# Kernel optimization log

Measured on AMD Instinct MI355X. Metric: run time of the kernel, lower is better.

## Reference

```python
import jax, jax.numpy as jnp
import numpy as np
from jax import lax

A_NUM = 2
N_LAYER = 4
DIM0 = 64   # fr_inner_dim_0 == signal_dim_0 (forced by view/squeeze logic)
DIM1 = 256  # fr_inner_dim_1
SD0 = 64
SD1 = 64
K_OUT = 8
UPS = 4
EPS = 1e-5
BSZ = 64


def setup_inputs() -> dict:
    key = jax.random.key(0)
    ks = jax.random.split(key, 16)
    s = 0.05
    f32 = jnp.float32
    inp = jax.random.normal(ks[0], (BSZ, 2, SD0, SD1), f32)
    # ComplexConv2d2 weights stored squeezed to their effective matmul form.
    W_in_r = jax.random.normal(ks[1], (DIM1 * A_NUM, SD1), f32) * s
    W_in_i = jax.random.normal(ks[2], (DIM1 * A_NUM, SD1), f32) * s
    W_pre_r = jax.random.normal(ks[3], (A_NUM,), f32) * s
    W_pre_i = jax.random.normal(ks[4], (A_NUM,), f32) * s
    Wm_r = jax.random.normal(ks[5], (2 * N_LAYER, SD0, SD0), f32) * s
    Wm_i = jax.random.normal(ks[6], (2 * N_LAYER, SD0, SD0), f32) * s
    Wc_r = jax.random.normal(ks[7], (N_LAYER, A_NUM), f32) * s
    Wc_i = jax.random.normal(ks[8], (N_LAYER, A_NUM), f32) * s
    W_l3_r = jax.random.normal(ks[9], (DIM0 * A_NUM, SD0), f32) * s
    W_l3_i = jax.random.normal(ks[10], (DIM0 * A_NUM, SD0), f32) * s
    conv1_w = jax.random.normal(ks[11], (N_LAYER, A_NUM, A_NUM, 3, 3), f32) * s
    conv2_w = jax.random.normal(ks[12], (N_LAYER, A_NUM, A_NUM, 3, 3), f32) * s
    bn1_g = jnp.ones((N_LAYER, A_NUM), f32)
    bn1_b = jnp.zeros((N_LAYER, A_NUM), f32)
    bn2_g = jnp.ones((N_LAYER, A_NUM), f32)
    bn2_b = jnp.zeros((N_LAYER, A_NUM), f32)
    W_out = jax.random.normal(ks[13], (A_NUM, 1, K_OUT, K_OUT), f32) * s
    return {"inp": inp, "W_in_r": W_in_r, "W_in_i": W_in_i, "W_pre_r": W_pre_r,
            "W_pre_i": W_pre_i, "Wm_r": Wm_r, "Wm_i": Wm_i, "Wc_r": Wc_r,
            "Wc_i": Wc_i, "W_l3_r": W_l3_r, "W_l3_i": W_l3_i,
            "conv1_w": conv1_w, "bn1_g": bn1_g, "bn1_b": bn1_b,
            "conv2_w": conv2_w, "bn2_g": bn2_g, "bn2_b": bn2_b, "W_out": W_out}


def _circ_conv(x, w):
    xp = jnp.pad(x, ((0, 0), (0, 0), (1, 1), (1, 1)), mode='wrap')
    return lax.conv_general_dilated(xp, w, (1, 1), 'VALID',
                                    dimension_numbers=('NCHW', 'OIHW', 'NCHW'))


def _bn(x, g, b):
    mu = jnp.mean(x, axis=(0, 2, 3), keepdims=True)
    var = jnp.var(x, axis=(0, 2, 3), keepdims=True)
    return (x - mu) * lax.rsqrt(var + EPS) * g[None, :, None, None] + b[None, :, None, None]


def _forward(inp, W_in_r, W_in_i, W_pre_r, W_pre_i, Wm_r, Wm_i, Wc_r, Wc_i,
             W_l3_r, W_l3_i, conv1_w, bn1_g, bn1_b, conv2_w, bn2_g, bn2_b, W_out):
    bsz = inp.shape[0]
    xr, xi = inp[:, 0], inp[:, 1]  # (b, sd0, sd1)
    # input_layer: complex conv, kernel (1, sd1) -> contraction over width
    yr = jnp.einsum('bhw,cw->bch', xr, W_in_r) - jnp.einsum('bhw,cw->bch', xi, W_in_i)
    yi = jnp.einsum('bhw,cw->bch', xi, W_in_r) + jnp.einsum('bhw,cw->bch', xr, W_in_i)
    xreal = yr.reshape(bsz, A_NUM, DIM1, DIM0).transpose(0, 1, 3, 2)  # (b,A,dim0,dim1)
    ximag = yi.reshape(bsz, A_NUM, DIM1, DIM0).transpose(0, 1, 3, 2)
    # concat_pre: complex 1x1 conv, A_NUM -> 1 channel
    x_real = (jnp.einsum('bahw,a->bhw', xreal, W_pre_r) - jnp.einsum('bahw,a->bhw', ximag, W_pre_i))[:, None]
    x_imag = (jnp.einsum('bahw,a->bhw', ximag, W_pre_r) + jnp.einsum('bahw,a->bhw', xreal, W_pre_i))[:, None]
    Gr, Gi = x_real, x_imag  # loop-invariant Gnk

    def phase_branch(xr_, xi_, Wr, Wi):
        a, c = xr_[:, 0], xi_[:, 0]  # (b, dim0, dim1)
        # complex conv kernel (sd0,1) == matmul over height
        Ir = (jnp.einsum('bhw,ch->bcw', a, Wr) - jnp.einsum('bhw,ch->bcw', c, Wi))[:, None]
        Ii = (jnp.einsum('bhw,ch->bcw', c, Wr) + jnp.einsum('bhw,ch->bcw', a, Wi))[:, None]
        s_ = 1.0 + jnp.log(Ir * Ir + Ii * Ii)
        EIr, EIi = s_ * Ir, -s_ * Ii
        ur, ui = Wr.T, Wi.T
        zr = jnp.einsum('hc,bncw->bnhw', ur, EIr) - jnp.einsum('hc,bncw->bnhw', ui, EIi)
        zi = jnp.einsum('hc,bncw->bnhw', ur, EIi) + jnp.einsum('hc,bncw->bnhw', ui, EIr)
        wr = jnp.sum(Gr * zr - Gi * zi, axis=3)  # (b,1,dim0)
        wi = jnp.sum(Gr * zi + Gi * zr, axis=3)
        ang = jnp.arctan2(wi, wr)[..., None]  # broadcast over dim1
        cr, ci = jnp.cos(ang), -jnp.sin(ang)
        return Gr * cr - Gi * ci, Gr * ci + Gi * cr

    for i in range(N_LAYER):
        x1r, x1i = phase_branch(x_real, x_imag, Wm_r[i], Wm_i[i])
        x2r, x2i = phase_branch(x_real, x_imag, Wm_r[i + N_LAYER], Wm_i[i + N_LAYER])
        sr = jnp.concatenate([x1r, x2r], 1)
        si = jnp.concatenate([x1i, x2i], 1)
        x_real = (jnp.einsum('bahw,a->bhw', sr, Wc_r[i]) - jnp.einsum('bahw,a->bhw', si, Wc_i[i]))[:, None]
        x_imag = (jnp.einsum('bahw,a->bhw', si, Wc_r[i]) + jnp.einsum('bahw,a->bhw', sr, Wc_i[i]))[:, None]

    # input_layer3: complex conv kernel (sd0,1), 1 -> dim0*A_NUM channels
    a, c = x_real[:, 0], x_imag[:, 0]
    fr = (jnp.einsum('bhw,ch->bcw', a, W_l3_r) - jnp.einsum('bhw,ch->bcw', c, W_l3_i)).reshape(bsz, -1)
    fi = (jnp.einsum('bhw,ch->bcw', c, W_l3_r) + jnp.einsum('bhw,ch->bcw', a, W_l3_i)).reshape(bsz, -1)
    m = jnp.max(jnp.sqrt(fr * fr + fi * fi), axis=1, keepdims=True)
    fr, fi = fr / m, fi / m
    fr = fr.reshape(bsz, A_NUM, DIM0, DIM1)
    fi = fi.reshape(bsz, A_NUM, DIM0, DIM1)
    x = jnp.sqrt(fr * fr + fi * fi)

    for i in range(N_LAYER):
        h = jax.nn.relu(_bn(_circ_conv(x, conv1_w[i]), bn1_g[i], bn1_b[i]))
        h = _bn(_circ_conv(h, conv2_w[i]), bn2_g[i], bn2_b[i])
        x = jax.nn.relu(x + h)

    # ConvTranspose2d(A_NUM, 1, K_OUT, stride=UPS, padding=2, output_padding=1)
    wt = jnp.flip(W_out, (2, 3)).transpose(1, 0, 2, 3)  # (1, A_NUM, k, k)
    pad_lo = K_OUT - 1 - 2
    pad_hi = pad_lo + 1
    y = lax.conv_general_dilated(x, wt, (1, 1),
                                 [(pad_lo, pad_hi), (pad_lo, pad_hi)],
                                 lhs_dilation=(UPS, UPS),
                                 dimension_numbers=('NCHW', 'OIHW', 'NCHW'))
    return y[:, 0]


def reference(inp, W_in_r, W_in_i, W_pre_r, W_pre_i, Wm_r, Wm_i, Wc_r, Wc_i,
              W_l3_r, W_l3_i, conv1_w, bn1_g, bn1_b, conv2_w, bn2_g, bn2_b, W_out):
    return _forward(inp, W_in_r, W_in_i, W_pre_r, W_pre_i, Wm_r, Wm_i, Wc_r, Wc_i,
                    W_l3_r, W_l3_i, conv1_w, bn1_g, bn1_b, conv2_w, bn2_g, bn2_b, W_out)
```

## Files before the change

kernel.cpp:

```cpp
#include <hip/hip_runtime.h>
#include <hip/hip_bf16.h>
#include <math.h>


__global__ void k0_prep(const float* __restrict__ Wr, const float* __restrict__ Wi,
                        const float* __restrict__ pr, const float* __restrict__ pi,
                        float* __restrict__ ArT, float* __restrict__ AiT,
                        float2* __restrict__ C) {
    int w  = blockIdx.x;
    int w2 = threadIdx.x;
    float p0r = pr[0], p1r = pr[1], p0i = pi[0], p1i = pi[1];
    float wr0 = Wr[w2 * 64 + w],         wi0 = Wi[w2 * 64 + w];
    float wr1 = Wr[(256 + w2) * 64 + w], wi1 = Wi[(256 + w2) * 64 + w];
    ArT[w * 256 + w2] = p0r * wr0 - p0i * wi0 + p1r * wr1 - p1i * wi1;
    AiT[w * 256 + w2] = p0r * wi0 + p0i * wr0 + p1r * wi1 + p1i * wr1;
    if (w2 < 64) C[w * 64 + w2] = make_float2(1.f, 0.f);
}

__global__ void k0b_T(const float* __restrict__ Wmr, const float* __restrict__ Wmi,
                      float* __restrict__ WmrT, float* __restrict__ WmiT) {
    int m = blockIdx.x;
    int t = threadIdx.x;
    const float* sr = Wmr + m * 4096;
    const float* si = Wmi + m * 4096;
    float* dr = WmrT + m * 4096;
    float* di = WmiT + m * 4096;
    for (int k = t; k < 4096; k += 256) {
        int c = k >> 6, h = k & 63;
        dr[h * 64 + c] = sr[k];
        di[h * 64 + c] = si[k];
    }
}

__global__ __launch_bounds__(256) void k1_G(const float* __restrict__ inp,
                                            const float* __restrict__ ArT,
                                            const float* __restrict__ AiT,
                                            float* __restrict__ Gr, float* __restrict__ Gi) {
    int hc = blockIdx.x;
    int b  = blockIdx.y;
    int t  = threadIdx.x;
    __shared__ float sxr[8][64], sxi[8][64];
    int base_r = (b * 2 + 0) * 4096 + hc * 8 * 64;
    int base_i = (b * 2 + 1) * 4096 + hc * 8 * 64;
    for (int k = t; k < 512; k += 256) {
        int r = k >> 6, w = k & 63;
        sxr[r][w] = inp[base_r + r * 64 + w];
        sxi[r][w] = inp[base_i + r * 64 + w];
    }
    __syncthreads();
    float accr[8], acci[8];
#pragma unroll
    for (int r = 0; r < 8; r++) { accr[r] = 0.f; acci[r] = 0.f; }
    for (int k = 0; k < 64; k++) {
        float ar = ArT[k * 256 + t], ai = AiT[k * 256 + t];
#pragma unroll
        for (int r = 0; r < 8; r++) {
            float xr = sxr[r][k], xi = sxi[r][k];
            accr[r] += xr * ar - xi * ai;
            acci[r] += xi * ar + xr * ai;
        }
    }
#pragma unroll
    for (int r = 0; r < 8; r++) {
        int h = hc * 8 + r;
        Gr[(b * 64 + h) * 256 + t] = accr[r];
        Gi[(b * 64 + h) * 256 + t] = acci[r];
    }
}

__global__ __launch_bounds__(1024) void k2_layer(const float* __restrict__ Gr,
                                                 const float* __restrict__ Gi,
                                                 const float2* __restrict__ C,
                                                 const float* __restrict__ Wmr,
                                                 const float* __restrict__ Wmi,
                                                 const float* __restrict__ WmrT,
                                                 const float* __restrict__ WmiT,
                                                 float2* __restrict__ wsum, int layer) {
    int wc = blockIdx.x;
    int j  = blockIdx.y;
    int b  = blockIdx.z;
    int t = threadIdx.x, tx = t & 63, ty = t >> 6;
    __shared__ float2 sX[4096];
    int mat = layer + 4 * j;
    int c0 = __builtin_amdgcn_readfirstlane(ty << 2);
    const float* Wr0  = Wmr  + mat * 4096 + c0 * 64;
    const float* Wi0  = Wmi  + mat * 4096 + c0 * 64;
    const float* WrT0 = WmrT + mat * 4096 + c0 * 64;
    const float* WiT0 = WmiT + mat * 4096 + c0 * 64;

    int gbase = b * 16384 + wc * 64 + tx;
    float gr_[4], gi_[4];
#pragma unroll
    for (int r = 0; r < 4; r++) {
        int h = (ty << 2) + r;
        float gr = Gr[gbase + h * 256], gi = Gi[gbase + h * 256];
        gr_[r] = gr; gi_[r] = gi;
        float2 c = C[b * 64 + h];
        sX[h * 64 + tx] = make_float2(c.x * gr - c.y * gi, c.x * gi + c.y * gr);
    }
    __syncthreads();

    float Ir[4] = {0.f, 0.f, 0.f, 0.f}, Ii[4] = {0.f, 0.f, 0.f, 0.f};
#pragma unroll 8
    for (int h = 0; h < 64; h++) {
        float2 x = sX[h * 64 + tx];
#pragma unroll
        for (int r = 0; r < 4; r++) {
            float wr = Wr0[r * 64 + h], wi = Wi0[r * 64 + h];
            Ir[r] += wr * x.x - wi * x.y;
            Ii[r] += wr * x.y + wi * x.x;
        }
    }
    __syncthreads();
#pragma unroll
    for (int r = 0; r < 4; r++) {
        float m2 = Ir[r] * Ir[r] + Ii[r] * Ii[r];
        float s = 1.f + __logf(m2);
        sX[((ty << 2) + r) * 64 + tx] = make_float2(s * Ir[r], -s * Ii[r]);
    }
    __syncthreads();

    float Zr[4] = {0.f, 0.f, 0.f, 0.f}, Zi[4] = {0.f, 0.f, 0.f, 0.f};
#pragma unroll 8
    for (int c = 0; c < 64; c++) {
        float2 e = sX[c * 64 + tx];
#pragma unroll
        for (int r = 0; r < 4; r++) {
            float wr = WrT0[r * 64 + c], wi = WiT0[r * 64 + c];
            Zr[r] += wr * e.x - wi * e.y;
            Zi[r] += wr * e.y + wi * e.x;
        }
    }
#pragma unroll
    for (int r = 0; r < 4; r++) {
        int h = (ty << 2) + r;
        float pr = gr_[r] * Zr[r] - gi_[r] * Zi[r];
        float pi = gr_[r] * Zi[r] + gi_[r] * Zr[r];
#pragma unroll
        for (int off = 32; off > 0; off >>= 1) {
            pr += __shfl_xor(pr, off);
            pi += __shfl_xor(pi, off);
        }
        if (tx == 0) wsum[((b * 64 + h) * 2 + j) * 4 + wc] = make_float2(pr, pi);
    }
}

__global__ void k3_cupdate(const float2* __restrict__ wsum, float2* __restrict__ C,
                           const float* __restrict__ Wcr, const float* __restrict__ Wci,
                           int layer) {
    int id = blockIdx.x * 256 + threadIdx.x;
    float accr = 0.f, acci = 0.f;
#pragma unroll
    for (int j = 0; j < 2; j++) {
        float wr = 0.f, wi = 0.f;
#pragma unroll
        for (int wc = 0; wc < 4; wc++) {
            float2 p = wsum[(id * 2 + j) * 4 + wc];
            wr += p.x; wi += p.y;
        }
        float m2 = wr * wr + wi * wi;
        float cr, ci;
        if (m2 > 0.f) {
            float inv = 1.f / sqrtf(m2);
            cr = wr * inv; ci = -wi * inv;
        } else { cr = 1.f; ci = 0.f; }
        float wcr = Wcr[layer * 2 + j], wci = Wci[layer * 2 + j];
        accr += cr * wcr - ci * wci;
        acci += ci * wcr + cr * wci;
    }
    C[id] = make_float2(accr, acci);
}

__global__ __launch_bounds__(1024) void k4_proj(const float* __restrict__ Gr,
                                                const float* __restrict__ Gi,
                                                const float2* __restrict__ C,
                                                const float* __restrict__ W3r,
                                                const float* __restrict__ W3i,
                                                float* __restrict__ xmag,
                                                float* __restrict__ pmax) {
    int wc = blockIdx.x;
    int cb = blockIdx.y;
    int b  = blockIdx.z;
    int t = threadIdx.x, tx = t & 63, ty = t >> 6;
    __shared__ float2 sX[4096];
    int c0 = __builtin_amdgcn_readfirstlane(ty << 2);
    const float* W3r0 = W3r + (cb * 64 + c0) * 64;
    const float* W3i0 = W3i + (cb * 64 + c0) * 64;
    int gbase = b * 16384 + wc * 64 + tx;
#pragma unroll
    for (int r = 0; r < 4; r++) {
        int h = (ty << 2) + r;
        float gr = Gr[gbase + h * 256], gi = Gi[gbase + h * 256];
        float2 c = C[b * 64 + h];
        sX[h * 64 + tx] = make_float2(c.x * gr - c.y * gi, c.x * gi + c.y * gr);
    }
    __syncthreads();
    float Fr[4] = {0.f, 0.f, 0.f, 0.f}, Fi[4] = {0.f, 0.f, 0.f, 0.f};
#pragma unroll 8
    for (int h = 0; h < 64; h++) {
        float2 x = sX[h * 64 + tx];
#pragma unroll
        for (int r = 0; r < 4; r++) {
            float wr = W3r0[r * 64 + h], wi = W3i0[r * 64 + h];
            Fr[r] += wr * x.x - wi * x.y;
            Fi[r] += wr * x.y + wi * x.x;
        }
    }
    float mx = 0.f;
#pragma unroll
    for (int r = 0; r < 4; r++) {
        int cl = (ty << 2) + r;
        float mag = sqrtf(Fr[r] * Fr[r] + Fi[r] * Fi[r]);
        xmag[(b * 128 + cb * 64 + cl) * 256 + wc * 64 + tx] = mag;
        mx = fmaxf(mx, mag);
    }
#pragma unroll
    for (int off = 32; off > 0; off >>= 1) mx = fmaxf(mx, __shfl_xor(mx, off));
    __syncthreads();
    float* scratch = (float*)sX;
    if (tx == 0) scratch[ty] = mx;
    __syncthreads();
    if (t == 0) {
        float m = scratch[0];
#pragma unroll
        for (int k = 1; k < 16; k++) m = fmaxf(m, scratch[k]);
        pmax[b * 8 + cb * 4 + wc] = m;
    }
}

__global__ void k5b_scale(float* __restrict__ x, const float* __restrict__ pmax) {
    int id = blockIdx.x * 256 + threadIdx.x;
    int b = id >> 15;
    float m = 0.f;
#pragma unroll
    for (int k = 0; k < 8; k++) m = fmaxf(m, pmax[b * 8 + k]);
    x[id] *= 1.f / m;
}

__global__ __launch_bounds__(256) void k_conv(const float* __restrict__ xin,
                                              const float* __restrict__ cw,
                                              const float* __restrict__ stats,
                                              float* __restrict__ hout,
                                              float* __restrict__ psum,
                                              float* __restrict__ psumsq,
                                              int layer, int apply_bn_relu) {
    int hb = blockIdx.x;
    int co = blockIdx.y;
    int b  = blockIdx.z;
    int tx = threadIdx.x;
    float wgt[18];
    const float* wp = cw + layer * 36 + co * 18;
#pragma unroll
    for (int k = 0; k < 18; k++) wgt[k] = wp[k];
    float sc0 = 1.f, sc1 = 1.f, sh0 = 0.f, sh1 = 0.f;
    if (apply_bn_relu) { sc0 = stats[0]; sc1 = stats[1]; sh0 = stats[2]; sh1 = stats[3]; }
    int wm = (tx + 255) & 255, wpp = (tx + 1) & 255;
    float lsum = 0.f, lsq = 0.f;
    for (int r = 0; r < 4; r++) {
        int hh = hb * 4 + r;
        int hm = (hh + 63) & 63, hp = (hh + 1) & 63;
        const int rows[3] = {hm, hh, hp};
        const int cols[3] = {wm, tx, wpp};
        float acc = 0.f;
#pragma unroll
        for (int ci = 0; ci < 2; ci++) {
            const float* xp = xin + (b * 2 + ci) * 16384;
            float sc = ci ? sc1 : sc0, sh = ci ? sh1 : sh0;
            const float* wg = wgt + ci * 9;
#pragma unroll
            for (int kh = 0; kh < 3; kh++)
#pragma unroll
                for (int kw = 0; kw < 3; kw++) {
                    float v = xp[rows[kh] * 256 + cols[kw]];
                    if (apply_bn_relu) v = fmaxf(v * sc + sh, 0.f);
                    acc += wg[kh * 3 + kw] * v;
                }
        }
        hout[((b * 2 + co) * 64 + hh) * 256 + tx] = acc;
        lsum += acc; lsq += acc * acc;
    }
#pragma unroll
    for (int off = 32; off > 0; off >>= 1) {
        lsum += __shfl_xor(lsum, off);
        lsq  += __shfl_xor(lsq, off);
    }
    __shared__ float ssum[4], ssq[4];
    int ty = tx >> 6, lane = tx & 63;
    if (lane == 0) { ssum[ty] = lsum; ssq[ty] = lsq; }
    __syncthreads();
    if (tx == 0) {
        int bl = b * 16 + hb;
        psum[co * 1024 + bl]   = ssum[0] + ssum[1] + ssum[2] + ssum[3];
        psumsq[co * 1024 + bl] = ssq[0] + ssq[1] + ssq[2] + ssq[3];
    }
}

__global__ void k_stats(const float* __restrict__ psum, const float* __restrict__ psumsq,
                        const float* __restrict__ g, const float* __restrict__ bb,
                        float* __restrict__ stats, int layer) {
    int ch = threadIdx.x >> 6, lane = threadIdx.x & 63;
    float s = 0.f, q = 0.f;
    for (int k = lane; k < 1024; k += 64) { s += psum[ch * 1024 + k]; q += psumsq[ch * 1024 + k]; }
#pragma unroll
    for (int off = 32; off > 0; off >>= 1) { s += __shfl_xor(s, off); q += __shfl_xor(q, off); }
    if (lane == 0) {
        const float N = 1048576.f;
        float mu = s / N;
        float var = q / N - mu * mu;
        float rs = rsqrtf(var + 1e-5f);
        float gamma = g[layer * 2 + ch];
        stats[ch]     = rs * gamma;
        stats[2 + ch] = bb[layer * 2 + ch] - mu * rs * gamma;
    }
}

__global__ void k8_res(float* __restrict__ x, const float* __restrict__ h2,
                       const float* __restrict__ stats) {
    int id = blockIdx.x * 256 + threadIdx.x;
    int ch = (id >> 14) & 1;
    float v = x[id] + h2[id] * stats[ch] + stats[2 + ch];
    x[id] = fmaxf(v, 0.f);
}

__global__ void k9_out(const float* __restrict__ x, const float* __restrict__ Wout,
                       float* __restrict__ out) {
    const int TOT = 64 * 257 * 1025;
    int id = blockIdx.x * 256 + threadIdx.x;
    if (id >= TOT) return;
    int b   = id / 263425;
    int rem = id - b * 263425;
    int oh  = rem / 1025;
    int ow  = rem - oh * 1025;
    int kh0 = (5 - oh) & 3;
    int kw0 = (5 - ow) & 3;
    float acc = 0.f;
#pragma unroll
    for (int ah = 0; ah < 2; ah++) {
        int kh = kh0 + 4 * ah;
        int d = oh + kh - 5;
        if (d < 0 || d > 252) continue;
        int rh = d >> 2;
#pragma unroll
        for (int aw = 0; aw < 2; aw++) {
            int kw = kw0 + 4 * aw;
            int e = ow + kw - 5;
            if (e < 0 || e > 1020) continue;
            int rw = e >> 2;
#pragma unroll
            for (int ci = 0; ci < 2; ci++) {
                float wv = Wout[ci * 64 + (7 - kh) * 8 + (7 - kw)];
                acc += wv * x[((b * 2 + ci) * 64 + rh) * 256 + rw];
            }
        }
    }
    out[id] = acc;
}

extern "C" void kernel_launch(void* const* d_in, const int* in_sizes, int n_in,
                              void* d_out, int out_size, void* d_ws, size_t ws_size,
                              hipStream_t stream) {
    const float* inp   = (const float*)d_in[0];
    const float* Winr  = (const float*)d_in[1];
    const float* Wini  = (const float*)d_in[2];
    const float* Wprer = (const float*)d_in[3];
    const float* Wprei = (const float*)d_in[4];
    const float* Wmr   = (const float*)d_in[5];
    const float* Wmi   = (const float*)d_in[6];
    const float* Wcr   = (const float*)d_in[7];
    const float* Wci   = (const float*)d_in[8];
    const float* W3r   = (const float*)d_in[9];
    const float* W3i   = (const float*)d_in[10];
    const float* cw1   = (const float*)d_in[11];
    const float* bn1g  = (const float*)d_in[12];
    const float* bn1b  = (const float*)d_in[13];
    const float* cw2   = (const float*)d_in[14];
    const float* bn2g  = (const float*)d_in[15];
    const float* bn2b  = (const float*)d_in[16];
    const float* Wout  = (const float*)d_in[17];
    float* out = (float*)d_out;

    float* ws = (float*)d_ws;
    float*  ArT   = ws;
    float*  AiT   = ArT + 16384;
    float2* C     = (float2*)(AiT + 16384);
    float*  Gr    = (float*)C + 8192;
    float*  Gi    = Gr + 1048576;
    float2* wsum  = (float2*)(Gi + 1048576);
    float*  xmag  = (float*)wsum + 65536;
    float*  h2    = xmag + 2097152;
    float*  pmax  = h2 + 2097152;
    float*  psum1 = pmax + 512;
    float*  psq1  = psum1 + 2048;
    float*  psum2 = psq1 + 2048;
    float*  psq2  = psum2 + 2048;
    float*  stats = psq2 + 2048;
    float*  h1    = Gr;
    float*  WmrT  = h2;
    float*  WmiT  = h2 + 32768;

    k0_prep<<<64, 256, 0, stream>>>(Winr, Wini, Wprer, Wprei, ArT, AiT, C);
    k0b_T<<<8, 256, 0, stream>>>(Wmr, Wmi, WmrT, WmiT);
    k1_G<<<dim3(8, 64), 256, 0, stream>>>(inp, ArT, AiT, Gr, Gi);
    for (int i = 0; i < 4; i++) {
        k2_layer<<<dim3(4, 2, 64), 1024, 0, stream>>>(Gr, Gi, C, Wmr, Wmi, WmrT, WmiT, wsum, i);
        k3_cupdate<<<16, 256, 0, stream>>>(wsum, C, Wcr, Wci, i);
    }
    k4_proj<<<dim3(4, 2, 64), 1024, 0, stream>>>(Gr, Gi, C, W3r, W3i, xmag, pmax);
    k5b_scale<<<8192, 256, 0, stream>>>(xmag, pmax);
    for (int i = 0; i < 4; i++) {
        k_conv<<<dim3(16, 2, 64), 256, 0, stream>>>(xmag, cw1, stats, h1, psum1, psq1, i, 0);
        k_stats<<<1, 128, 0, stream>>>(psum1, psq1, bn1g, bn1b, stats, i);
        k_conv<<<dim3(16, 2, 64), 256, 0, stream>>>(h1, cw2, stats, h2, psum2, psq2, i, 1);
        k_stats<<<1, 128, 0, stream>>>(psum2, psq2, bn2g, bn2b, stats + 4, i);
        k8_res<<<8192, 256, 0, stream>>>(xmag, h2, stats + 4);
    }
    k9_out<<<65857, 256, 0, stream>>>(xmag, Wout, out);
}
```

Before: 591.0 us.

## Fuse scale and residual passes into conv kernels; merge k2 matrix pair per block

The separate max-normalisation kernel and the per-layer residual+ReLU kernel are removed. Their arithmetic is now applied on the fly where the next conv1 or the final transposed conv reads the activations, and conv1 writes the updated x into a ping-pong buffer that borrows the output array as scratch. k2_layer now processes both Wm matrices (j loop) in one 512-thread block with 8 rows per thread and a second shared buffer, so each G tile is loaded once instead of twice. The aim is to cut elementwise memory passes and kernel launches, at the cost of extra global reads inside the 3x3 stencil (the residual term is recomputed per tap) and higher register pressure in k2.

```diff
diff --git a/kernel.cpp b/kernel.cpp
--- a/kernel.cpp
+++ b/kernel.cpp
@@ -68,31 +68,26 @@
     }
 }
 
-__global__ __launch_bounds__(1024) void k2_layer(const float* __restrict__ Gr,
-                                                 const float* __restrict__ Gi,
-                                                 const float2* __restrict__ C,
-                                                 const float* __restrict__ Wmr,
-                                                 const float* __restrict__ Wmi,
-                                                 const float* __restrict__ WmrT,
-                                                 const float* __restrict__ WmiT,
-                                                 float2* __restrict__ wsum, int layer) {
+__global__ __launch_bounds__(512) void k2_layer(const float* __restrict__ Gr,
+                                                const float* __restrict__ Gi,
+                                                const float2* __restrict__ C,
+                                                const float* __restrict__ Wmr,
+                                                const float* __restrict__ Wmi,
+                                                const float* __restrict__ WmrT,
+                                                const float* __restrict__ WmiT,
+                                                float2* __restrict__ wsum, int layer) {
     int wc = blockIdx.x;
-    int j  = blockIdx.y;
-    int b  = blockIdx.z;
+    int b  = blockIdx.y;
     int t = threadIdx.x, tx = t & 63, ty = t >> 6;
     __shared__ float2 sX[4096];
-    int mat = layer + 4 * j;
-    int c0 = __builtin_amdgcn_readfirstlane(ty << 2);
-    const float* Wr0  = Wmr  + mat * 4096 + c0 * 64;
-    const float* Wi0  = Wmi  + mat * 4096 + c0 * 64;
-    const float* WrT0 = WmrT + mat * 4096 + c0 * 64;
-    const float* WiT0 = WmiT + mat * 4096 + c0 * 64;
+    __shared__ float2 sE[4096];
+    int h0 = __builtin_amdgcn_readfirstlane(ty << 3);
 
     int gbase = b * 16384 + wc * 64 + tx;
-    float gr_[4], gi_[4];
-#pragma unroll
-    for (int r = 0; r < 4; r++) {
-        int h = (ty << 2) + r;
+    float gr_[8], gi_[8];
+#pragma unroll
+    for (int r = 0; r < 8; r++) {
+        int h = h0 + r;
         float gr = Gr[gbase + h * 256], gi = Gi[gbase + h * 256];
         gr_[r] = gr; gi_[r] = gi;
         float2 c = C[b * 64 + h];
@@ -100,48 +95,56 @@
     }
     __syncthreads();
 
-    float Ir[4] = {0.f, 0.f, 0.f, 0.f}, Ii[4] = {0.f, 0.f, 0.f, 0.f};
-#pragma unroll 8
-    for (int h = 0; h < 64; h++) {
-        float2 x = sX[h * 64 + tx];
-#pragma unroll
-        for (int r = 0; r < 4; r++) {
-            float wr = Wr0[r * 64 + h], wi = Wi0[r * 64 + h];
-            Ir[r] += wr * x.x - wi * x.y;
-            Ii[r] += wr * x.y + wi * x.x;
-        }
-    }
-    __syncthreads();
-#pragma unroll
-    for (int r = 0; r < 4; r++) {
-        float m2 = Ir[r] * Ir[r] + Ii[r] * Ii[r];
-        float s = 1.f + __logf(m2);
-        sX[((ty << 2) + r) * 64 + tx] = make_float2(s * Ir[r], -s * Ii[r]);
-    }
-    __syncthreads();
-
-    float Zr[4] = {0.f, 0.f, 0.f, 0.f}, Zi[4] = {0.f, 0.f, 0.f, 0.f};
-#pragma unroll 8
-    for (int c = 0; c < 64; c++) {
-        float2 e = sX[c * 64 + tx];
-#pragma unroll
-        for (int r = 0; r < 4; r++) {
-            float wr = WrT0[r * 64 + c], wi = WiT0[r * 64 + c];
-            Zr[r] += wr * e.x - wi * e.y;
-            Zi[r] += wr * e.y + wi * e.x;
-        }
-    }
-#pragma unroll
-    for (int r = 0; r < 4; r++) {
-        int h = (ty << 2) + r;
-        float pr = gr_[r] * Zr[r] - gi_[r] * Zi[r];
-        float pi = gr_[r] * Zi[r] + gi_[r] * Zr[r];
-#pragma unroll
-        for (int off = 32; off > 0; off >>= 1) {
-            pr += __shfl_xor(pr, off);
-            pi += __shfl_xor(pi, off);
-        }
-        if (tx == 0) wsum[((b * 64 + h) * 2 + j) * 4 + wc] = make_float2(pr, pi);
+    for (int j = 0; j < 2; j++) {
+        int mat = layer + 4 * j;
+        const float* Wr0  = Wmr  + mat * 4096 + h0 * 64;
+        const float* Wi0  = Wmi  + mat * 4096 + h0 * 64;
+        const float* WrT0 = WmrT + mat * 4096 + h0 * 64;
+        const float* WiT0 = WmiT + mat * 4096 + h0 * 64;
+
+        float Ir[8] = {0,0,0,0,0,0,0,0}, Ii[8] = {0,0,0,0,0,0,0,0};
+#pragma unroll 4
+        for (int h = 0; h < 64; h++) {
+            float2 x = sX[h * 64 + tx];
+#pragma unroll
+            for (int r = 0; r < 8; r++) {
+                float wr = Wr0[r * 64 + h], wi = Wi0[r * 64 + h];
+                Ir[r] += wr * x.x - wi * x.y;
+                Ii[r] += wr * x.y + wi * x.x;
+            }
+        }
+#pragma unroll
+        for (int r = 0; r < 8; r++) {
+            float m2 = Ir[r] * Ir[r] + Ii[r] * Ii[r];
+            float s = 1.f + __logf(m2);
+            sE[(h0 + r) * 64 + tx] = make_float2(s * Ir[r], -s * Ii[r]);
+        }
+        __syncthreads();
+
+        float Zr[8] = {0,0,0,0,0,0,0,0}, Zi[8] = {0,0,0,0,0,0,0,0};
+#pragma unroll 4
+        for (int c = 0; c < 64; c++) {
+            float2 e = sE[c * 64 + tx];
+#pragma unroll
+            for (int r = 0; r < 8; r++) {
+                float wr = WrT0[r * 64 + c], wi = WiT0[r * 64 + c];
+                Zr[r] += wr * e.x - wi * e.y;
+                Zi[r] += wr * e.y + wi * e.x;
+            }
+        }
+#pragma unroll
+        for (int r = 0; r < 8; r++) {
+            int h = h0 + r;
+            float pr = gr_[r] * Zr[r] - gi_[r] * Zi[r];
+            float pi = gr_[r] * Zi[r] + gi_[r] * Zr[r];
+#pragma unroll
+            for (int off = 32; off > 0; off >>= 1) {
+                pr += __shfl_xor(pr, off);
+                pi += __shfl_xor(pi, off);
+            }
+            if (tx == 0) wsum[((b * 64 + h) * 2 + j) * 4 + wc] = make_float2(pr, pi);
+        }
+        __syncthreads();
     }
 }
 
@@ -195,7 +198,7 @@
         sX[h * 64 + tx] = make_float2(c.x * gr - c.y * gi, c.x * gi + c.y * gr);
     }
     __syncthreads();
-    float Fr[4] = {0.f, 0.f, 0.f, 0.f}, Fi[4] = {0.f, 0.f, 0.f, 0.f};
+    float Fr[4] = {0,0,0,0}, Fi[4] = {0,0,0,0};
 #pragma unroll 8
     for (int h = 0; h < 64; h++) {
         float2 x = sX[h * 64 + tx];
@@ -228,22 +231,16 @@
     }
 }
 
-__global__ void k5b_scale(float* __restrict__ x, const float* __restrict__ pmax) {
-    int id = blockIdx.x * 256 + threadIdx.x;
-    int b = id >> 15;
-    float m = 0.f;
-#pragma unroll
-    for (int k = 0; k < 8; k++) m = fmaxf(m, pmax[b * 8 + k]);
-    x[id] *= 1.f / m;
-}
-
-__global__ __launch_bounds__(256) void k_conv(const float* __restrict__ xin,
-                                              const float* __restrict__ cw,
-                                              const float* __restrict__ stats,
-                                              float* __restrict__ hout,
-                                              float* __restrict__ psum,
-                                              float* __restrict__ psumsq,
-                                              int layer, int apply_bn_relu) {
+__global__ __launch_bounds__(256) void k_conv1f(const float* __restrict__ xin,
+                                                const float* __restrict__ h2,
+                                                const float* __restrict__ cw,
+                                                const float* __restrict__ stats2,
+                                                const float* __restrict__ pmax,
+                                                float* __restrict__ hout,
+                                                float* __restrict__ xout,
+                                                float* __restrict__ psum,
+                                                float* __restrict__ psumsq,
+                                                int layer) {
     int hb = blockIdx.x;
     int co = blockIdx.y;
     int b  = blockIdx.z;
@@ -252,8 +249,15 @@
     const float* wp = cw + layer * 36 + co * 18;
 #pragma unroll
     for (int k = 0; k < 18; k++) wgt[k] = wp[k];
-    float sc0 = 1.f, sc1 = 1.f, sh0 = 0.f, sh1 = 0.f;
-    if (apply_bn_relu) { sc0 = stats[0]; sc1 = stats[1]; sh0 = stats[2]; sh1 = stats[3]; }
+    float sc0 = 0.f, sc1 = 0.f, sh0 = 0.f, sh1 = 0.f, inv = 1.f;
+    if (layer == 0) {
+        float m = 0.f;
+#pragma unroll
+        for (int k = 0; k < 8; k++) m = fmaxf(m, pmax[b * 8 + k]);
+        inv = 1.f / m;
+    } else {
+        sc0 = stats2[0]; sc1 = stats2[1]; sh0 = stats2[2]; sh1 = stats2[3];
+    }
     int wm = (tx + 255) & 255, wpp = (tx + 1) & 255;
     float lsum = 0.f, lsq = 0.f;
     for (int r = 0; r < 4; r++) {
@@ -264,15 +268,20 @@
         float acc = 0.f;
 #pragma unroll
         for (int ci = 0; ci < 2; ci++) {
-            const float* xp = xin + (b * 2 + ci) * 16384;
+            const float* xp  = xin + (b * 2 + ci) * 16384;
+            const float* hp2 = h2  + (b * 2 + ci) * 16384;
             float sc = ci ? sc1 : sc0, sh = ci ? sh1 : sh0;
             const float* wg = wgt + ci * 9;
 #pragma unroll
             for (int kh = 0; kh < 3; kh++)
 #pragma unroll
                 for (int kw = 0; kw < 3; kw++) {
-                    float v = xp[rows[kh] * 256 + cols[kw]];
-                    if (apply_bn_relu) v = fmaxf(v * sc + sh, 0.f);
+                    int idx = rows[kh] * 256 + cols[kw];
+                    float v;
+                    if (layer == 0) v = xp[idx] * inv;
+                    else            v = fmaxf(xp[idx] + hp2[idx] * sc + sh, 0.f);
+                    if (ci == co && kh == 1 && kw == 1)
+                        xout[(b * 2 + co) * 16384 + hh * 256 + tx] = v;
                     acc += wg[kh * 3 + kw] * v;
                 }
         }
@@ -285,8 +294,64 @@
         lsq  += __shfl_xor(lsq, off);
     }
     __shared__ float ssum[4], ssq[4];
-    int ty = tx >> 6, lane = tx & 63;
-    if (lane == 0) { ssum[ty] = lsum; ssq[ty] = lsq; }
+    int tyy = tx >> 6, lane = tx & 63;
+    if (lane == 0) { ssum[tyy] = lsum; ssq[tyy] = lsq; }
+    __syncthreads();
+    if (tx == 0) {
+        int bl = b * 16 + hb;
+        psum[co * 1024 + bl]   = ssum[0] + ssum[1] + ssum[2] + ssum[3];
+        psumsq[co * 1024 + bl] = ssq[0] + ssq[1] + ssq[2] + ssq[3];
+    }
+}
+
+__global__ __launch_bounds__(256) void k_conv2(const float* __restrict__ h1,
+                                               const float* __restrict__ cw,
+                                               const float* __restrict__ stats1,
+                                               float* __restrict__ hout,
+                                               float* __restrict__ psum,
+                                               float* __restrict__ psumsq,
+                                               int layer) {
+    int hb = blockIdx.x;
+    int co = blockIdx.y;
+    int b  = blockIdx.z;
+    int tx = threadIdx.x;
+    float wgt[18];
+    const float* wp = cw + layer * 36 + co * 18;
+#pragma unroll
+    for (int k = 0; k < 18; k++) wgt[k] = wp[k];
+    float sc0 = stats1[0], sc1 = stats1[1], sh0 = stats1[2], sh1 = stats1[3];
+    int wm = (tx + 255) & 255, wpp = (tx + 1) & 255;
+    float lsum = 0.f, lsq = 0.f;
+    for (int r = 0; r < 4; r++) {
+        int hh = hb * 4 + r;
+        int hm = (hh + 63) & 63, hp = (hh + 1) & 63;
+        const int rows[3] = {hm, hh, hp};
+        const int cols[3] = {wm, tx, wpp};
+        float acc = 0.f;
+#pragma unroll
+        for (int ci = 0; ci < 2; ci++) {
+            const float* xp = h1 + (b * 2 + ci) * 16384;
+            float sc = ci ? sc1 : sc0, sh = ci ? sh1 : sh0;
+            const float* wg = wgt + ci * 9;
+#pragma unroll
+            for (int kh = 0; kh < 3; kh++)
+#pragma unroll
+                for (int kw = 0; kw < 3; kw++) {
+                    float v = fmaxf(xp[rows[kh] * 256 + cols[kw]] * sc + sh, 0.f);
+                    acc += wg[kh * 3 + kw] * v;
+                }
+        }
+        hout[((b * 2 + co) * 64 + hh) * 256 + tx] = acc;
+        lsum += acc; lsq += acc * acc;
+    }
+#pragma unroll
+    for (int off = 32; off > 0; off >>= 1) {
+        lsum += __shfl_xor(lsum, off);
+        lsq  += __shfl_xor(lsq, off);
+    }
+    __shared__ float ssum[4], ssq[4];
+    int tyy = tx >> 6, lane = tx & 63;
+    if (lane == 0) { ssum[tyy] = lsum; ssq[tyy] = lsq; }
     __syncthreads();
     if (tx == 0) {
         int bl = b * 16 + hb;
@@ -314,15 +379,8 @@
     }
 }
 
-__global__ void k8_res(float* __restrict__ x, const float* __restrict__ h2,
-                       const float* __restrict__ stats) {
-    int id = blockIdx.x * 256 + threadIdx.x;
-    int ch = (id >> 14) & 1;
-    float v = x[id] + h2[id] * stats[ch] + stats[2 + ch];
-    x[id] = fmaxf(v, 0.f);
-}
-
-__global__ void k9_out(const float* __restrict__ x, const float* __restrict__ Wout,
+__global__ void k9_out(const float* __restrict__ x3, const float* __restrict__ h2,
+                       const float* __restrict__ stats2, const float* __restrict__ Wout,
                        float* __restrict__ out) {
     const int TOT = 64 * 257 * 1025;
     int id = blockIdx.x * 256 + threadIdx.x;
@@ -333,6 +391,7 @@
     int ow  = rem - oh * 1025;
     int kh0 = (5 - oh) & 3;
     int kw0 = (5 - ow) & 3;
+    float sc0 = stats2[0], sc1 = stats2[1], sh0 = stats2[2], sh1 = stats2[3];
     float acc = 0.f;
 #pragma unroll
     for (int ah = 0; ah < 2; ah++) {
@@ -348,8 +407,10 @@
             int rw = e >> 2;
 #pragma unroll
             for (int ci = 0; ci < 2; ci++) {
+                int idx = ((b * 2 + ci) * 64 + rh) * 256 + rw;
+                float v = fmaxf(x3[idx] + h2[idx] * (ci ? sc1 : sc0) + (ci ? sh1 : sh0), 0.f);
                 float wv = Wout[ci * 64 + (7 - kh) * 8 + (7 - kw)];
-                acc += wv * x[((b * 2 + ci) * 64 + rh) * 256 + rw];
+                acc += wv * v;
             }
         }
     }
@@ -397,22 +458,26 @@
     float*  h1    = Gr;
     float*  WmrT  = h2;
     float*  WmiT  = h2 + 32768;
+    float*  outS  = out;
 
     k0_prep<<<64, 256, 0, stream>>>(Winr, Wini, Wprer, Wprei, ArT, AiT, C);
     k0b_T<<<8, 256, 0, stream>>>(Wmr, Wmi, WmrT, WmiT);
     k1_G<<<dim3(8, 64), 256, 0, stream>>>(inp, ArT, AiT, Gr, Gi);
     for (int i = 0; i < 4; i++) {
-        k2_layer<<<dim3(4, 2, 64), 1024, 0, stream>>>(Gr, Gi, C, Wmr, Wmi, WmrT, WmiT, wsum, i);
+        k2_layer<<<dim3(4, 64), 512, 0, stream>>>(Gr, Gi, C, Wmr, Wmi, WmrT, WmiT, wsum, i);
         k3_cupdate<<<16, 256, 0, stream>>>(wsum, C, Wcr, Wci, i);
     }
     k4_proj<<<dim3(4, 2, 64), 1024, 0, stream>>>(Gr, Gi, C, W3r, W3i, xmag, pmax);
-    k5b_scale<<<8192, 256, 0, stream>>>(xmag, pmax);
+
+    float* xbuf[5] = {xmag, outS, xmag, outS, xmag};
     for (int i = 0; i < 4; i++) {
-        k_conv<<<dim3(16, 2, 64), 256, 0, stream>>>(xmag, cw1, stats, h1, psum1, psq1, i, 0);
+        const float* xin = xbuf[i];
+        float* xout = xbuf[i + 1];
+        k_conv1f<<<dim3(16, 2, 64), 256, 0, stream>>>(xin, h2, cw1, stats + 4, pmax,
+                                                      h1, xout, psum1, psq1, i);
         k_stats<<<1, 128, 0, stream>>>(psum1, psq1, bn1g, bn1b, stats, i);
-        k_conv<<<dim3(16, 2, 64), 256, 0, stream>>>(h1, cw2, stats, h2, psum2, psq2, i, 1);
+        k_conv2<<<dim3(16, 2, 64), 256, 0, stream>>>(h1, cw2, stats, h2, psum2, psq2, i);
         k_stats<<<1, 128, 0, stream>>>(psum2, psq2, bn2g, bn2b, stats + 4, i);
-        k8_res<<<8192, 256, 0, stream>>>(xmag, h2, stats + 4);
-    }
-    k9_out<<<65857, 256, 0, stream>>>(xmag, Wout, out);
-}
+    }
+    k9_out<<<65857, 256, 0, stream>>>(xmag, h2, stats + 4, Wout, out);
+}
```

Result: slower. 667.8 us (+13.0%).
